# Performance work log

Measured on AMD Instinct MI355X. Metric: run time of the kernel, lower is better.

Reference implementation:

```python
import jax, jax.numpy as jnp
import numpy as np

N_NODES = 100000
N_EDGES = 1600000
N_SUP = 2
IN_DIM = 256
OUT_DIM = 64


def setup_inputs() -> dict:
    key = jax.random.key(0)
    k1, k2, k3, k4, k5 = jax.random.split(key, 5)
    x = jax.random.normal(k1, (N_NODES, IN_DIM), dtype=jnp.float32)
    W = jax.random.normal(k2, (N_SUP, IN_DIM, OUT_DIM), dtype=jnp.float32) * 0.05
    edge_val = jax.random.uniform(k3, (N_SUP, N_EDGES), dtype=jnp.float32)
    edge_src = jax.random.randint(k4, (N_SUP, N_EDGES), 0, N_NODES)
    edge_dst = jax.random.randint(k5, (N_SUP, N_EDGES), 0, N_NODES)
    return {"x": x, "W": W, "edge_val": edge_val,
            "edge_src": edge_src, "edge_dst": edge_dst}


def _spmm(val, src, dst, dense):
    # sparse (COO) @ dense: gather rows by src, scale by edge value, scatter-add to dst
    msg = dense[src] * val[:, None]                      # [E, out]
    return jax.ops.segment_sum(msg, dst, num_segments=N_NODES)  # [N, out]


def reference(x, W, edge_val, edge_src, edge_dst):
    out = jnp.zeros((N_NODES, OUT_DIM), dtype=x.dtype)
    for i in range(N_SUP):  # small fixed number of supports
        pre_sup = x @ W[i]                               # [N, out]
        out = out + _spmm(edge_val[i], edge_src[i], edge_dst[i], pre_sup)
    return jax.nn.relu(out)
```

## Files before the change

### kernel.cpp

```cpp
#include <hip/hip_runtime.h>

#define N_NODES 100000
#define N_EDGES 1600000
#define N_SUP 2
#define IN_DIM 256
#define OUT_DIM 64
#define N_TOT_EDGES (N_SUP * N_EDGES)
#define GM 64
#define NBLK ((N_NODES + GM - 1) / GM)

#define SHIFT 7
#define BUCKN 128
#define NBUCK ((N_NODES + BUCKN - 1) / BUCKN)
#define CAP 4608
#define CHUNK 4096
#define BGRID ((N_TOT_EDGES + CHUNK - 1) / CHUNK)

typedef __attribute__((ext_vector_type(8))) short short8;
typedef __attribute__((ext_vector_type(4))) float floatx4;
typedef unsigned long long u64;

__device__ inline ushort f2bf(float f) {
    unsigned u = __float_as_uint(f);
    return (ushort)((u + 0x7fffu + ((u >> 16) & 1u)) >> 16);
}
__device__ inline float bf2f(ushort h) {
    return __uint_as_float(((unsigned)h) << 16);
}

__global__ __launch_bounds__(256) void wb_kernel(
    const float* __restrict__ W, ushort* __restrict__ Wb,
    int* __restrict__ bcur)
{
    int idx = blockIdx.x * 256 + threadIdx.x;
    if (idx < NBUCK) bcur[idx] = idx * CAP;
    int j    = idx & 7;
    int lane = (idx >> 3) & 63;
    int nt   = (idx >> 9) & 7;
    int ks   = idx >> 12;
    int k = ks * 32 + (lane >> 4) * 8 + j;
    int n = nt * 16 + (lane & 15);
    Wb[idx] = f2bf(W[((size_t)(n >> 6) * IN_DIM + k) * OUT_DIM + (n & 63)]);
}

__global__ __launch_bounds__(256) void gemm_kernel(
    const float* __restrict__ x, const ushort* __restrict__ Wb,
    ushort* __restrict__ psb)
{
    __shared__ __align__(16) ushort xs[GM][264];
    const int row0 = blockIdx.x * GM;
    const int trow = threadIdx.x >> 6;
    const int tcol = threadIdx.x & 63;

#pragma unroll
    for (int j = 0; j < 16; ++j) {
        int r = j * 4 + trow;
        int gr = row0 + r;
        if (gr > N_NODES - 1) gr = N_NODES - 1;
        float4 v = ((const float4*)x)[(size_t)gr * 64 + tcol];
        ushort4 h;
        h.x = f2bf(v.x); h.y = f2bf(v.y); h.z = f2bf(v.z); h.w = f2bf(v.w);
        *(ushort4*)&xs[r][tcol * 4] = h;
    }
    __syncthreads();

    const int wave = threadIdx.x >> 6;
    const int lane = threadIdx.x & 63;
    const int q = lane >> 4;
    const int m = lane & 15;
    const int nt0 = wave * 2;

    floatx4 acc[4][2];
#pragma unroll
    for (int mt = 0; mt < 4; ++mt)
#pragma unroll
        for (int nt = 0; nt < 2; ++nt)
            acc[mt][nt] = (floatx4){0.f, 0.f, 0.f, 0.f};

    const short8* Wbv = (const short8*)Wb;
#pragma unroll
    for (int ks = 0; ks < 8; ++ks) {
        short8 b0 = Wbv[((ks * 8) + nt0) * 64 + lane];
        short8 b1 = Wbv[((ks * 8) + nt0 + 1) * 64 + lane];
#pragma unroll
        for (int mt = 0; mt < 4; ++mt) {
            short8 a = *(const short8*)&xs[mt * 16 + m][ks * 32 + q * 8];
            acc[mt][0] = __builtin_amdgcn_mfma_f32_16x16x32_bf16(a, b0, acc[mt][0], 0, 0, 0);
            acc[mt][1] = __builtin_amdgcn_mfma_f32_16x16x32_bf16(a, b1, acc[mt][1], 0, 0, 0);
        }
    }

#pragma unroll
    for (int mt = 0; mt < 4; ++mt) {
#pragma unroll
        for (int nt = 0; nt < 2; ++nt) {
            int col = wave * 32 + nt * 16 + m;
            int sup = col >> 6, ch = col & 63;
#pragma unroll
            for (int r = 0; r < 4; ++r) {
                int row = row0 + mt * 16 + q * 4 + r;
                if (row < N_NODES)
                    psb[((size_t)sup * N_NODES + row) * OUT_DIM + ch] =
                        f2bf(acc[mt][nt][r]);
            }
        }
    }
}

__global__ __launch_bounds__(256) void bin_kernel(
    const int* __restrict__ edge_src, const int* __restrict__ edge_dst,
    const float* __restrict__ edge_val,
    int* __restrict__ bcur, u64* __restrict__ sbuf)
{
    __shared__ int hist[NBUCK], gbase[NBUCK];
    const int base = blockIdx.x * CHUNK + threadIdx.x;

    u64 pk[16];
    int bk[16];
    int rk[16];
    for (int i = threadIdx.x; i < NBUCK; i += 256) hist[i] = 0;
    __syncthreads();

#pragma unroll
    for (int j = 0; j < 16; ++j) {
        int gid = base + j * 256;
        bk[j] = -1;
        if (gid < N_TOT_EDGES) {
            int dst = edge_dst[gid];
            int src = edge_src[gid];
            float val = edge_val[gid];
            int srcsup = (gid >= N_EDGES ? N_NODES : 0) + src;
            bk[j] = dst >> SHIFT;
            pk[j] = ((u64)__float_as_uint(val) << 32)
                  | (u64)(((unsigned)srcsup << SHIFT) | (unsigned)(dst & (BUCKN - 1)));
            rk[j] = atomicAdd(&hist[bk[j]], 1);
        }
    }
    __syncthreads();
    for (int i = threadIdx.x; i < NBUCK; i += 256) {
        int h = hist[i];
        gbase[i] = h ? atomicAdd(&bcur[i], h) : 0;
    }
    __syncthreads();
#pragma unroll
    for (int j = 0; j < 16; ++j) {
        if (bk[j] >= 0) {
            size_t pos = (size_t)gbase[bk[j]] + rk[j];
            if (pos < (size_t)(bk[j] + 1) * CAP)
                sbuf[pos] = pk[j];
        }
    }
}

__global__ __launch_bounds__(512) void fused_kernel(
    const ushort* __restrict__ psb, const u64* __restrict__ sbuf,
    const int* __restrict__ bcur, float* __restrict__ out)
{
    __shared__ u64 srec[CAP];
    __shared__ int h[BUCKN], sc[BUCKN], eb[BUCKN];
    const int b = blockIdx.x;
    const int tid = threadIdx.x;

    int cnt = bcur[b] - b * CAP;
    if (cnt > CAP) cnt = CAP;
    const u64* sb = sbuf + (size_t)b * CAP;

    if (tid < BUCKN) h[tid] = 0;
    __syncthreads();

    u64 pk[9];
    int rk[9];
#pragma unroll
    for (int jj = 0; jj < 9; ++jj) {
        int i = tid + jj * 512;
        rk[jj] = -1;
        if (i < cnt) {
            pk[jj] = sb[i];
            rk[jj] = atomicAdd(&h[(int)(pk[jj] & (BUCKN - 1))], 1);
        }
    }
    __syncthreads();

    if (tid < BUCKN) sc[tid] = h[tid];
    __syncthreads();
    for (int off = 1; off < BUCKN; off <<= 1) {
        int add = (tid < BUCKN && tid >= off) ? sc[tid - off] : 0;
        __syncthreads();
        if (tid < BUCKN) sc[tid] += add;
        __syncthreads();
    }
    if (tid < BUCKN) eb[tid] = sc[tid] - h[tid];
    __syncthreads();

#pragma unroll
    for (int jj = 0; jj < 9; ++jj) {
        if (rk[jj] >= 0) {
            int node = (int)(pk[jj] & (BUCKN - 1));
            srec[eb[node] + rk[jj]] = pk[jj];
        }
    }
    __syncthreads();

    const int wave = tid >> 6;
    const int lane = tid & 63;
    const int grp  = lane >> 4;
    const int cl   = lane & 15;
    const int nbase = b << SHIFT;

    for (int t = 0; t < 16; ++t) {
        const int d = wave * 16 + t;
        const int e = sc[d];
        const int s = e - h[d];
        float4 acc = {0.f, 0.f, 0.f, 0.f};

        for (int jb = s; jb < e; jb += 16) {
            int i0 = jb + grp, i1 = jb + 4 + grp, i2 = jb + 8 + grp, i3 = jb + 12 + grp;
            u64 r0 = 0, r1 = 0, r2 = 0, r3 = 0;
            if (i0 < e) r0 = srec[i0];
            if (i1 < e) r1 = srec[i1];
            if (i2 < e) r2 = srec[i2];
            if (i3 < e) r3 = srec[i3];
            float v0 = __uint_as_float((unsigned)(r0 >> 32));
            float v1 = __uint_as_float((unsigned)(r1 >> 32));
            float v2 = __uint_as_float((unsigned)(r2 >> 32));
            float v3 = __uint_as_float((unsigned)(r3 >> 32));
            unsigned w0 = (unsigned)r0 >> SHIFT;
            unsigned w1 = (unsigned)r1 >> SHIFT;
            unsigned w2 = (unsigned)r2 >> SHIFT;
            unsigned w3 = (unsigned)r3 >> SHIFT;
            ushort4 p0 = *(const ushort4*)&psb[(size_t)w0 * OUT_DIM + cl * 4];
            ushort4 p1 = *(const ushort4*)&psb[(size_t)w1 * OUT_DIM + cl * 4];
            ushort4 p2 = *(const ushort4*)&psb[(size_t)w2 * OUT_DIM + cl * 4];
            ushort4 p3 = *(const ushort4*)&psb[(size_t)w3 * OUT_DIM + cl * 4];
            acc.x = fmaf(bf2f(p0.x), v0, acc.x);
            acc.y = fmaf(bf2f(p0.y), v0, acc.y);
            acc.z = fmaf(bf2f(p0.z), v0, acc.z);
            acc.w = fmaf(bf2f(p0.w), v0, acc.w);
            acc.x = fmaf(bf2f(p1.x), v1, acc.x);
            acc.y = fmaf(bf2f(p1.y), v1, acc.y);
            acc.z = fmaf(bf2f(p1.z), v1, acc.z);
            acc.w = fmaf(bf2f(p1.w), v1, acc.w);
            acc.x = fmaf(bf2f(p2.x), v2, acc.x);
            acc.y = fmaf(bf2f(p2.y), v2, acc.y);
            acc.z = fmaf(bf2f(p2.z), v2, acc.z);
            acc.w = fmaf(bf2f(p2.w), v2, acc.w);
            acc.x = fmaf(bf2f(p3.x), v3, acc.x);
            acc.y = fmaf(bf2f(p3.y), v3, acc.y);
            acc.z = fmaf(bf2f(p3.z), v3, acc.z);
            acc.w = fmaf(bf2f(p3.w), v3, acc.w);
        }

        acc.x += __shfl_xor(acc.x, 16); acc.x += __shfl_xor(acc.x, 32);
        acc.y += __shfl_xor(acc.y, 16); acc.y += __shfl_xor(acc.y, 32);
        acc.z += __shfl_xor(acc.z, 16); acc.z += __shfl_xor(acc.z, 32);
        acc.w += __shfl_xor(acc.w, 16); acc.w += __shfl_xor(acc.w, 32);

        const int node = nbase + d;
        if (lane < 16 && node < N_NODES) {
            acc.x = fmaxf(acc.x, 0.f); acc.y = fmaxf(acc.y, 0.f);
            acc.z = fmaxf(acc.z, 0.f); acc.w = fmaxf(acc.w, 0.f);
            ((float4*)out)[(size_t)node * 16 + cl] = acc;
        }
    }
}

extern "C" void kernel_launch(void* const* d_in, const int* in_sizes, int n_in,
                              void* d_out, int out_size, void* d_ws, size_t ws_size,
                              hipStream_t stream)
{
    const float* x        = (const float*)d_in[0];
    const float* W        = (const float*)d_in[1];
    const float* edge_val = (const float*)d_in[2];
    const int*   edge_src = (const int*)d_in[3];
    const int*   edge_dst = (const int*)d_in[4];
    float* out = (float*)d_out;

    ushort* psb = (ushort*)d_ws;
    char* p = (char*)d_ws;
    u64*  sbuf = (u64*)(p + 25600000);
    int*  bcur = (int*)(p + 54427648);
    ushort* Wb = (ushort*)(p + 54431232);

    wb_kernel<<<128, 256, 0, stream>>>(W, Wb, bcur);
    gemm_kernel<<<NBLK, 256, 0, stream>>>(x, Wb, psb);
    bin_kernel<<<BGRID, 256, 0, stream>>>(edge_src, edge_dst, edge_val,
                                          bcur, sbuf);
    fused_kernel<<<NBUCK, 512, 0, stream>>>(psb, sbuf, bcur, out);
}
```

Measured before the change: 321.5 us.

## Merge GEMM and edge binning into one launch; unroll gather loop to 32 edges

The GEMM and edge-binning kernels are combined into a single launch, with block index deciding which role a block takes and both roles sharing one shared-memory buffer. This lets the compute-bound GEMM blocks and the memory/atomic-bound binning blocks run concurrently and drops one kernel launch boundary. The SpMM gather loop in the fused kernel now handles 32 edges per iteration instead of 16, putting more independent row loads in flight. The cost is higher register pressure in the gather loop and shared memory sized for the larger of the two roles.

Result: faster. 300.1 us (-6.7%).

```diff
diff --git a/kernel.cpp b/kernel.cpp
--- a/kernel.cpp
+++ b/kernel.cpp
@@ -43,111 +43,114 @@
     Wb[idx] = f2bf(W[((size_t)(n >> 6) * IN_DIM + k) * OUT_DIM + (n & 63)]);
 }
 
-__global__ __launch_bounds__(256) void gemm_kernel(
+__global__ __launch_bounds__(256) void gb_kernel(
     const float* __restrict__ x, const ushort* __restrict__ Wb,
-    ushort* __restrict__ psb)
-{
-    __shared__ __align__(16) ushort xs[GM][264];
-    const int row0 = blockIdx.x * GM;
-    const int trow = threadIdx.x >> 6;
-    const int tcol = threadIdx.x & 63;
-
-#pragma unroll
-    for (int j = 0; j < 16; ++j) {
-        int r = j * 4 + trow;
-        int gr = row0 + r;
-        if (gr > N_NODES - 1) gr = N_NODES - 1;
-        float4 v = ((const float4*)x)[(size_t)gr * 64 + tcol];
-        ushort4 h;
-        h.x = f2bf(v.x); h.y = f2bf(v.y); h.z = f2bf(v.z); h.w = f2bf(v.w);
-        *(ushort4*)&xs[r][tcol * 4] = h;
-    }
-    __syncthreads();
-
-    const int wave = threadIdx.x >> 6;
-    const int lane = threadIdx.x & 63;
-    const int q = lane >> 4;
-    const int m = lane & 15;
-    const int nt0 = wave * 2;
-
-    floatx4 acc[4][2];
-#pragma unroll
-    for (int mt = 0; mt < 4; ++mt)
-#pragma unroll
-        for (int nt = 0; nt < 2; ++nt)
-            acc[mt][nt] = (floatx4){0.f, 0.f, 0.f, 0.f};
-
-    const short8* Wbv = (const short8*)Wb;
-#pragma unroll
-    for (int ks = 0; ks < 8; ++ks) {
-        short8 b0 = Wbv[((ks * 8) + nt0) * 64 + lane];
-        short8 b1 = Wbv[((ks * 8) + nt0 + 1) * 64 + lane];
-#pragma unroll
-        for (int mt = 0; mt < 4; ++mt) {
-            short8 a = *(const short8*)&xs[mt * 16 + m][ks * 32 + q * 8];
-            acc[mt][0] = __builtin_amdgcn_mfma_f32_16x16x32_bf16(a, b0, acc[mt][0], 0, 0, 0);
-            acc[mt][1] = __builtin_amdgcn_mfma_f32_16x16x32_bf16(a, b1, acc[mt][1], 0, 0, 0);
-        }
-    }
-
-#pragma unroll
-    for (int mt = 0; mt < 4; ++mt) {
-#pragma unroll
-        for (int nt = 0; nt < 2; ++nt) {
-            int col = wave * 32 + nt * 16 + m;
-            int sup = col >> 6, ch = col & 63;
-#pragma unroll
-            for (int r = 0; r < 4; ++r) {
-                int row = row0 + mt * 16 + q * 4 + r;
-                if (row < N_NODES)
-                    psb[((size_t)sup * N_NODES + row) * OUT_DIM + ch] =
-                        f2bf(acc[mt][nt][r]);
-            }
-        }
-    }
-}
-
-__global__ __launch_bounds__(256) void bin_kernel(
+    ushort* __restrict__ psb,
     const int* __restrict__ edge_src, const int* __restrict__ edge_dst,
     const float* __restrict__ edge_val,
     int* __restrict__ bcur, u64* __restrict__ sbuf)
 {
-    __shared__ int hist[NBUCK], gbase[NBUCK];
-    const int base = blockIdx.x * CHUNK + threadIdx.x;
-
-    u64 pk[16];
-    int bk[16];
-    int rk[16];
-    for (int i = threadIdx.x; i < NBUCK; i += 256) hist[i] = 0;
-    __syncthreads();
-
-#pragma unroll
-    for (int j = 0; j < 16; ++j) {
-        int gid = base + j * 256;
-        bk[j] = -1;
-        if (gid < N_TOT_EDGES) {
-            int dst = edge_dst[gid];
-            int src = edge_src[gid];
-            float val = edge_val[gid];
-            int srcsup = (gid >= N_EDGES ? N_NODES : 0) + src;
-            bk[j] = dst >> SHIFT;
-            pk[j] = ((u64)__float_as_uint(val) << 32)
-                  | (u64)(((unsigned)srcsup << SHIFT) | (unsigned)(dst & (BUCKN - 1)));
-            rk[j] = atomicAdd(&hist[bk[j]], 1);
-        }
-    }
-    __syncthreads();
-    for (int i = threadIdx.x; i < NBUCK; i += 256) {
-        int h = hist[i];
-        gbase[i] = h ? atomicAdd(&bcur[i], h) : 0;
-    }
-    __syncthreads();
-#pragma unroll
-    for (int j = 0; j < 16; ++j) {
-        if (bk[j] >= 0) {
-            size_t pos = (size_t)gbase[bk[j]] + rk[j];
-            if (pos < (size_t)(bk[j] + 1) * CAP)
-                sbuf[pos] = pk[j];
+    __shared__ __align__(16) char smem[GM * 264 * 2];
+
+    if (blockIdx.x < NBLK) {
+        ushort (*xs)[264] = (ushort (*)[264])smem;
+        const int row0 = blockIdx.x * GM;
+        const int trow = threadIdx.x >> 6;
+        const int tcol = threadIdx.x & 63;
+
+#pragma unroll
+        for (int j = 0; j < 16; ++j) {
+            int r = j * 4 + trow;
+            int gr = row0 + r;
+            if (gr > N_NODES - 1) gr = N_NODES - 1;
+            float4 v = ((const float4*)x)[(size_t)gr * 64 + tcol];
+            ushort4 h;
+            h.x = f2bf(v.x); h.y = f2bf(v.y); h.z = f2bf(v.z); h.w = f2bf(v.w);
+            *(ushort4*)&xs[r][tcol * 4] = h;
+        }
+        __syncthreads();
+
+        const int wave = threadIdx.x >> 6;
+        const int lane = threadIdx.x & 63;
+        const int q = lane >> 4;
+        const int m = lane & 15;
+        const int nt0 = wave * 2;
+
+        floatx4 acc[4][2];
+#pragma unroll
+        for (int mt = 0; mt < 4; ++mt)
+#pragma unroll
+            for (int nt = 0; nt < 2; ++nt)
+                acc[mt][nt] = (floatx4){0.f, 0.f, 0.f, 0.f};
+
+        const short8* Wbv = (const short8*)Wb;
+#pragma unroll
+        for (int ks = 0; ks < 8; ++ks) {
+            short8 b0 = Wbv[((ks * 8) + nt0) * 64 + lane];
+            short8 b1 = Wbv[((ks * 8) + nt0 + 1) * 64 + lane];
+#pragma unroll
+            for (int mt = 0; mt < 4; ++mt) {
+                short8 a = *(const short8*)&xs[mt * 16 + m][ks * 32 + q * 8];
+                acc[mt][0] = __builtin_amdgcn_mfma_f32_16x16x32_bf16(a, b0, acc[mt][0], 0, 0, 0);
+                acc[mt][1] = __builtin_amdgcn_mfma_f32_16x16x32_bf16(a, b1, acc[mt][1], 0, 0, 0);
+            }
+        }
+
+#pragma unroll
+        for (int mt = 0; mt < 4; ++mt) {
+#pragma unroll
+            for (int nt = 0; nt < 2; ++nt) {
+                int col = wave * 32 + nt * 16 + m;
+                int sup = col >> 6, ch = col & 63;
+#pragma unroll
+                for (int r = 0; r < 4; ++r) {
+                    int row = row0 + mt * 16 + q * 4 + r;
+                    if (row < N_NODES)
+                        psb[((size_t)sup * N_NODES + row) * OUT_DIM + ch] =
+                            f2bf(acc[mt][nt][r]);
+                }
+            }
+        }
+    } else {
+        int* hist  = (int*)smem;
+        int* gbase = hist + NBUCK;
+        const int bb = blockIdx.x - NBLK;
+        const int base = bb * CHUNK + threadIdx.x;
+
+        u64 pk[16];
+        int bk[16];
+        int rk[16];
+        for (int i = threadIdx.x; i < NBUCK; i += 256) hist[i] = 0;
+        __syncthreads();
+
+#pragma unroll
+        for (int j = 0; j < 16; ++j) {
+            int gid = base + j * 256;
+            bk[j] = -1;
+            if (gid < N_TOT_EDGES) {
+                int dst = edge_dst[gid];
+                int src = edge_src[gid];
+                float val = edge_val[gid];
+                int srcsup = (gid >= N_EDGES ? N_NODES : 0) + src;
+                bk[j] = dst >> SHIFT;
+                pk[j] = ((u64)__float_as_uint(val) << 32)
+                      | (u64)(((unsigned)srcsup << SHIFT) | (unsigned)(dst & (BUCKN - 1)));
+                rk[j] = atomicAdd(&hist[bk[j]], 1);
+            }
+        }
+        __syncthreads();
+        for (int i = threadIdx.x; i < NBUCK; i += 256) {
+            int h = hist[i];
+            gbase[i] = h ? atomicAdd(&bcur[i], h) : 0;
+        }
+        __syncthreads();
+#pragma unroll
+        for (int j = 0; j < 16; ++j) {
+            if (bk[j] >= 0) {
+                size_t pos = (size_t)gbase[bk[j]] + rk[j];
+                if (pos < (size_t)(bk[j] + 1) * CAP)
+                    sbuf[pos] = pk[j];
+            }
         }
     }
 }
@@ -213,25 +216,44 @@
         const int s = e - h[d];
         float4 acc = {0.f, 0.f, 0.f, 0.f};
 
-        for (int jb = s; jb < e; jb += 16) {
-            int i0 = jb + grp, i1 = jb + 4 + grp, i2 = jb + 8 + grp, i3 = jb + 12 + grp;
-            u64 r0 = 0, r1 = 0, r2 = 0, r3 = 0;
+        for (int jb = s; jb < e; jb += 32) {
+            int i0 = jb + grp,      i1 = jb + 4 + grp;
+            int i2 = jb + 8 + grp,  i3 = jb + 12 + grp;
+            int i4 = jb + 16 + grp, i5 = jb + 20 + grp;
+            int i6 = jb + 24 + grp, i7 = jb + 28 + grp;
+            u64 r0 = 0, r1 = 0, r2 = 0, r3 = 0, r4 = 0, r5 = 0, r6 = 0, r7 = 0;
             if (i0 < e) r0 = srec[i0];
             if (i1 < e) r1 = srec[i1];
             if (i2 < e) r2 = srec[i2];
             if (i3 < e) r3 = srec[i3];
+            if (i4 < e) r4 = srec[i4];
+            if (i5 < e) r5 = srec[i5];
+            if (i6 < e) r6 = srec[i6];
+            if (i7 < e) r7 = srec[i7];
             float v0 = __uint_as_float((unsigned)(r0 >> 32));
             float v1 = __uint_as_float((unsigned)(r1 >> 32));
             float v2 = __uint_as_float((unsigned)(r2 >> 32));
             float v3 = __uint_as_float((unsigned)(r3 >> 32));
+            float v4 = __uint_as_float((unsigned)(r4 >> 32));
+            float v5 = __uint_as_float((unsigned)(r5 >> 32));
+            float v6 = __uint_as_float((unsigned)(r6 >> 32));
+            float v7 = __uint_as_float((unsigned)(r7 >> 32));
             unsigned w0 = (unsigned)r0 >> SHIFT;
             unsigned w1 = (unsigned)r1 >> SHIFT;
             unsigned w2 = (unsigned)r2 >> SHIFT;
             unsigned w3 = (unsigned)r3 >> SHIFT;
+            unsigned w4 = (unsigned)r4 >> SHIFT;
+            unsigned w5 = (unsigned)r5 >> SHIFT;
+            unsigned w6 = (unsigned)r6 >> SHIFT;
+            unsigned w7 = (unsigned)r7 >> SHIFT;
             ushort4 p0 = *(const ushort4*)&psb[(size_t)w0 * OUT_DIM + cl * 4];
             ushort4 p1 = *(const ushort4*)&psb[(size_t)w1 * OUT_DIM + cl * 4];
             ushort4 p2 = *(const ushort4*)&psb[(size_t)w2 * OUT_DIM + cl * 4];
             ushort4 p3 = *(const ushort4*)&psb[(size_t)w3 * OUT_DIM + cl * 4];
+            ushort4 p4 = *(const ushort4*)&psb[(size_t)w4 * OUT_DIM + cl * 4];
+            ushort4 p5 = *(const ushort4*)&psb[(size_t)w5 * OUT_DIM + cl * 4];
+            ushort4 p6 = *(const ushort4*)&psb[(size_t)w6 * OUT_DIM + cl * 4];
+            ushort4 p7 = *(const ushort4*)&psb[(size_t)w7 * OUT_DIM + cl * 4];
             acc.x = fmaf(bf2f(p0.x), v0, acc.x);
             acc.y = fmaf(bf2f(p0.y), v0, acc.y);
             acc.z = fmaf(bf2f(p0.z), v0, acc.z);
@@ -248,6 +270,22 @@
             acc.y = fmaf(bf2f(p3.y), v3, acc.y);
             acc.z = fmaf(bf2f(p3.z), v3, acc.z);
             acc.w = fmaf(bf2f(p3.w), v3, acc.w);
+            acc.x = fmaf(bf2f(p4.x), v4, acc.x);
+            acc.y = fmaf(bf2f(p4.y), v4, acc.y);
+            acc.z = fmaf(bf2f(p4.z), v4, acc.z);
+            acc.w = fmaf(bf2f(p4.w), v4, acc.w);
+            acc.x = fmaf(bf2f(p5.x), v5, acc.x);
+            acc.y = fmaf(bf2f(p5.y), v5, acc.y);
+            acc.z = fmaf(bf2f(p5.z), v5, acc.z);
+            acc.w = fmaf(bf2f(p5.w), v5, acc.w);
+            acc.x = fmaf(bf2f(p6.x), v6, acc.x);
+            acc.y = fmaf(bf2f(p6.y), v6, acc.y);
+            acc.z = fmaf(bf2f(p6.z), v6, acc.z);
+            acc.w = fmaf(bf2f(p6.w), v6, acc.w);
+            acc.x = fmaf(bf2f(p7.x), v7, acc.x);
+            acc.y = fmaf(bf2f(p7.y), v7, acc.y);
+            acc.z = fmaf(bf2f(p7.z), v7, acc.z);
+            acc.w = fmaf(bf2f(p7.w), v7, acc.w);
         }
 
         acc.x += __shfl_xor(acc.x, 16); acc.x += __shfl_xor(acc.x, 32);
@@ -282,8 +320,8 @@
     ushort* Wb = (ushort*)(p + 54431232);
 
     wb_kernel<<<128, 256, 0, stream>>>(W, Wb, bcur);
-    gemm_kernel<<<NBLK, 256, 0, stream>>>(x, Wb, psb);
-    bin_kernel<<<BGRID, 256, 0, stream>>>(edge_src, edge_dst, edge_val,
-                                          bcur, sbuf);
+    gb_kernel<<<NBLK + BGRID, 256, 0, stream>>>(x, Wb, psb,
+                                                edge_src, edge_dst, edge_val,
+                                                bcur, sbuf);
     fused_kernel<<<NBUCK, 512, 0, stream>>>(psb, sbuf, bcur, out);
 }
```
